# Performance work log

Hardware: AMD Instinct MI355X
Metric: run time of the kernel (lower is better)

## Reference

```python
import jax, jax.numpy as jnp
import numpy as np

N = 100000      # num_nodes
E = 1600000     # num_edges (avg degree 16)
D_IN, D_H, D_OUT = 128, 128, 64


def _glorot(key, shape):
    fan_in = shape[0]
    bound = 1.0 / np.sqrt(fan_in)
    return jax.random.uniform(key, shape, jnp.float32, -bound, bound)


def setup_inputs() -> dict:
    key = jax.random.key(0)
    ks = jax.random.split(key, 9)
    x = jax.random.normal(ks[0], (N, D_IN), jnp.float32)
    edge_index = jax.random.randint(ks[1], (2, E), 0, N, jnp.int32)
    # SAGEConv layer 1: lin_l (aggregated, with bias) and lin_r (root, no bias)
    W1l = _glorot(ks[2], (D_IN, D_H))
    b1 = jnp.zeros((D_H,), jnp.float32)
    W1r = _glorot(ks[3], (D_IN, D_H))
    # SAGEConv layer 2
    W2l = _glorot(ks[4], (D_H, D_OUT))
    b2 = jnp.zeros((D_OUT,), jnp.float32)
    W2r = _glorot(ks[5], (D_H, D_OUT))
    return {"x": x, "W1l": W1l, "b1": b1, "W1r": W1r,
            "W2l": W2l, "b2": b2, "W2r": W2r, "edge_index": edge_index}


def _sage_conv(x, edge_index, Wl, b, Wr):
    """PyG SAGEConv with mean aggregation: out = mean_{j in N(i)} x_j @ Wl + b + x_i @ Wr."""
    src, dst = edge_index[0], edge_index[1]
    msg_sum = jax.ops.segment_sum(x[src], dst, num_segments=N)          # [N, d_in]
    deg = jax.ops.segment_sum(jnp.ones((src.shape[0],), x.dtype), dst,
                              num_segments=N)                            # [N]
    mean = msg_sum / jnp.maximum(deg, 1.0)[:, None]
    return mean @ Wl + b + x @ Wr


def reference(x, W1l, b1, W1r, W2l, b2, W2r, edge_index):
    h = jax.nn.relu(_sage_conv(x, edge_index, W1l, b1, W1r))
    # dropout is identity at inference (training=False)
    return _sage_conv(h, edge_index, W2l, b2, W2r)
```

## Files before the change

### kernel.cpp

```cpp
#include <hip/hip_runtime.h>

#define NODES 100000
#define NEDGE 1600000
#define NPART 8
#define PSIZE (NODES / NPART)
#define EW 48

typedef _Float16 half8 __attribute__((ext_vector_type(8)));
typedef float floatx4 __attribute__((ext_vector_type(4)));
typedef float floatx2 __attribute__((ext_vector_type(2)));
typedef int intx4 __attribute__((ext_vector_type(4)));


static __device__ __forceinline__ unsigned int packh2(float a, float b) {
    union { _Float16 h; unsigned short s; } x, y;
    x.h = (_Float16)a; y.h = (_Float16)b;
    return (unsigned int)x.s | ((unsigned int)y.s << 16);
}
static __device__ __forceinline__ float2 unpackh2(unsigned int u) {
    union { unsigned short s; _Float16 h; } x, y;
    x.s = (unsigned short)(u & 0xffffu);
    y.s = (unsigned short)(u >> 16);
    return make_float2((float)x.h, (float)y.h);
}


template <bool HI>
static __device__ __forceinline__ float2 fp8x2_to_f32(unsigned int u) {
    floatx2 r = __builtin_amdgcn_cvt_pk_f32_fp8(u, HI);
    return make_float2(r.x, r.y);
}
static __device__ __forceinline__ unsigned int pack4fp8(float a, float b,
                                                        float c, float d) {
    unsigned int w = (unsigned int)__builtin_amdgcn_cvt_pk_fp8_f32(a, b, 0, false);
    w = (unsigned int)__builtin_amdgcn_cvt_pk_fp8_f32(c, d, (int)w, true);
    return w;
}


static __global__ __launch_bounds__(256) void prep_kernel(
    const float* __restrict__ W1l, const float* __restrict__ W1r,
    const float* __restrict__ W2l, const float* __restrict__ W2r,
    _Float16* __restrict__ WT1, _Float16* __restrict__ WT2,
    int* __restrict__ cnt) {
    int bid = blockIdx.x;
    if (bid < 192) {
        int idx = bid * 256 + threadIdx.x;
        if (idx < 256 * 128) {
            int n = idx >> 7, k = idx & 127;
            float v = (n < 128) ? W1l[k * 128 + n] : W1r[k * 128 + (n - 128)];
            WT1[n * 128 + k] = (_Float16)v;
        } else if (idx < 256 * 128 + 128 * 128) {
            int i2 = idx - 256 * 128;
            int n = i2 >> 7, k = i2 & 127;
            float v = (n < 64) ? W2l[k * 64 + n] : W2r[k * 64 + (n - 64)];
            WT2[n * 128 + k] = (_Float16)v;
        }
    } else {
        int i = (bid - 192) * 256 + threadIdx.x;
        int stride = 128 * 256;
        for (; i < NODES; i += stride) cnt[i] = 0;
    }
}


static __global__ __launch_bounds__(256) void build_ell_kernel(
    const int* __restrict__ src, const int* __restrict__ dst,
    int* __restrict__ cnt, int* __restrict__ colE) {
    const int part = blockIdx.x & (NPART - 1);
    const int lo = part * PSIZE;
    const int hi = lo + PSIZE;
    const int group = blockIdx.x >> 3;
    const int ngroups = gridDim.x >> 3;
    const int NV = NEDGE / 4;
    const intx4* dst4 = (const intx4*)dst;
    const intx4* src4 = (const intx4*)src;
    int i = group * 256 + threadIdx.x;
    int stride = ngroups * 256;
    for (int e4 = i; e4 < NV; e4 += stride) {
        intx4 d4 = __builtin_nontemporal_load(dst4 + e4);
        intx4 s4 = __builtin_nontemporal_load(src4 + e4);
#pragma unroll
        for (int q = 0; q < 4; ++q) {
            int d = d4[q];
            if (d >= lo && d < hi) {
                int pos = atomicAdd(&cnt[d], 1);
                if (pos < EW) colE[(size_t)d * EW + pos] = s4[q];
            }
        }
    }
}


static __global__ __launch_bounds__(256) void gemm1_mfma_kernel(
    const float* __restrict__ X, const _Float16* __restrict__ WT1,
    const float* __restrict__ b1,
    unsigned char* __restrict__ U8, _Float16* __restrict__ V16) {
    __shared__ _Float16 sX[64][136];
    const int tid = threadIdx.x;
    const int row0 = blockIdx.x * 64;
    {
        int c4 = (tid & 31) * 4;
        int r0 = tid >> 5;
#pragma unroll
        for (int p = 0; p < 8; ++p) {
            int r = r0 + p * 8;
            int row = row0 + r;
            float4 v = make_float4(0.f, 0.f, 0.f, 0.f);
            if (row < NODES) v = *(const float4*)(X + (size_t)row * 128 + c4);
            sX[r][c4 + 0] = (_Float16)v.x;
            sX[r][c4 + 1] = (_Float16)v.y;
            sX[r][c4 + 2] = (_Float16)v.z;
            sX[r][c4 + 3] = (_Float16)v.w;
        }
    }
    __syncthreads();

    const int wave = tid >> 6;
    const int lane = tid & 63;
    const int l15 = lane & 15;
    const int quad = lane >> 4;

    floatx4 acc[4][4];
#pragma unroll
    for (int j = 0; j < 4; ++j)
#pragma unroll
        for (int m = 0; m < 4; ++m) acc[j][m] = (floatx4){0.f, 0.f, 0.f, 0.f};

    const _Float16* Wbase = WT1 + (size_t)(wave * 64 + l15) * 128 + quad * 8;

    for (int k0 = 0; k0 < 128; k0 += 32) {
        half8 a[4];
#pragma unroll
        for (int m = 0; m < 4; ++m)
            a[m] = *(const half8*)&sX[m * 16 + l15][quad * 8 + k0];
#pragma unroll
        for (int j = 0; j < 4; ++j) {
            half8 b = *(const half8*)(Wbase + (size_t)j * 16 * 128 + k0);
#pragma unroll
            for (int m = 0; m < 4; ++m)
                acc[j][m] = __builtin_amdgcn_mfma_f32_16x16x32_f16(b, a[m], acc[j][m], 0, 0, 0);
        }
    }

    if (wave < 2) {
#pragma unroll
        for (int j = 0; j < 4; ++j) {
            int n0 = wave * 64 + j * 16 + quad * 4;
#pragma unroll
            for (int m = 0; m < 4; ++m) {
                int node = row0 + m * 16 + l15;
                if (node < NODES) {
                    unsigned int w = pack4fp8(acc[j][m][0], acc[j][m][1],
                                              acc[j][m][2], acc[j][m][3]);
                    *(unsigned int*)(U8 + (size_t)node * 128 + n0) = w;
                }
            }
        }
    } else {
#pragma unroll
        for (int j = 0; j < 4; ++j) {
            int nn0 = (wave - 2) * 64 + j * 16 + quad * 4;
            float4 bb = *(const float4*)(b1 + nn0);
#pragma unroll
            for (int m = 0; m < 4; ++m) {
                int node = row0 + m * 16 + l15;
                if (node < NODES) {
                    uint2 o;
                    o.x = packh2(acc[j][m][0] + bb.x, acc[j][m][1] + bb.y);
                    o.y = packh2(acc[j][m][2] + bb.z, acc[j][m][3] + bb.w);
                    *(uint2*)(V16 + (size_t)node * 128 + nn0) = o;
                }
            }
        }
    }
}


static __global__ __launch_bounds__(256) void agg1_kernel(
    const unsigned char* __restrict__ U8, const int* __restrict__ cnt,
    const int* __restrict__ colE, unsigned int* __restrict__ H32) {
    int node = (int)((blockIdx.x * 256 + threadIdx.x) >> 6);
    int lane = threadIdx.x & 63;
    if (node >= NODES) return;
    const int g = lane >> 4;
    const int l16 = lane & 15;
    int dcnt = cnt[node];
    if (dcnt > EW) dcnt = EW;
    int s = node * EW;
    int e = s + dcnt;
    float inv = 1.0f / (float)max(dcnt, 1);

    float acc[8];
#pragma unroll
    for (int i = 0; i < 8; ++i) acc[i] = 0.f;

    int p = s + g;
    for (; p + 12 < e; p += 16) {
        int c0 = colE[p], c1 = colE[p + 4], c2 = colE[p + 8], c3 = colE[p + 12];
        uint2 u0 = *(const uint2*)(U8 + (size_t)c0 * 128 + l16 * 8);
        uint2 u1 = *(const uint2*)(U8 + (size_t)c1 * 128 + l16 * 8);
        uint2 u2 = *(const uint2*)(U8 + (size_t)c2 * 128 + l16 * 8);
        uint2 u3 = *(const uint2*)(U8 + (size_t)c3 * 128 + l16 * 8);
#pragma unroll
        for (int q = 0; q < 4; ++q) {
            uint2 u = (q == 0) ? u0 : (q == 1) ? u1 : (q == 2) ? u2 : u3;
            float2 a0 = fp8x2_to_f32<false>(u.x), a1 = fp8x2_to_f32<true>(u.x);
            float2 a2 = fp8x2_to_f32<false>(u.y), a3 = fp8x2_to_f32<true>(u.y);
            acc[0] += a0.x; acc[1] += a0.y; acc[2] += a1.x; acc[3] += a1.y;
            acc[4] += a2.x; acc[5] += a2.y; acc[6] += a3.x; acc[7] += a3.y;
        }
    }
    for (; p < e; p += 4) {
        uint2 u = *(const uint2*)(U8 + (size_t)colE[p] * 128 + l16 * 8);
        float2 a0 = fp8x2_to_f32<false>(u.x), a1 = fp8x2_to_f32<true>(u.x);
        float2 a2 = fp8x2_to_f32<false>(u.y), a3 = fp8x2_to_f32<true>(u.y);
        acc[0] += a0.x; acc[1] += a0.y; acc[2] += a1.x; acc[3] += a1.y;
        acc[4] += a2.x; acc[5] += a2.y; acc[6] += a3.x; acc[7] += a3.y;
    }

#pragma unroll
    for (int i = 0; i < 8; ++i) {
        acc[i] += __shfl_xor(acc[i], 16);
        acc[i] += __shfl_xor(acc[i], 32);
    }

    if (lane < 16) {
        uint4 vv = *(const uint4*)(H32 + (size_t)node * 64 + l16 * 4);
        float2 v0 = unpackh2(vv.x), v1 = unpackh2(vv.y);
        float2 v2 = unpackh2(vv.z), v3 = unpackh2(vv.w);
        uint4 o;
        o.x = packh2(fmaxf(acc[0] * inv + v0.x, 0.f), fmaxf(acc[1] * inv + v0.y, 0.f));
        o.y = packh2(fmaxf(acc[2] * inv + v1.x, 0.f), fmaxf(acc[3] * inv + v1.y, 0.f));
        o.z = packh2(fmaxf(acc[4] * inv + v2.x, 0.f), fmaxf(acc[5] * inv + v2.y, 0.f));
        o.w = packh2(fmaxf(acc[6] * inv + v3.x, 0.f), fmaxf(acc[7] * inv + v3.y, 0.f));
        *(uint4*)(H32 + (size_t)node * 64 + l16 * 4) = o;
    }
}


static __global__ __launch_bounds__(256) void gemm2_mfma_kernel(
    const _Float16* __restrict__ H16, const _Float16* __restrict__ WT2,
    const float* __restrict__ b2,
    _Float16* __restrict__ T16, float* __restrict__ OUT) {
    __shared__ _Float16 sX[64][136];
    const int tid = threadIdx.x;
    const int row0 = blockIdx.x * 64;
    {
        int c8 = (tid & 15) * 8;
        int r0 = tid >> 4;
#pragma unroll
        for (int p = 0; p < 4; ++p) {
            int r = r0 + p * 16;
            int row = row0 + r;
            uint4 v = make_uint4(0u, 0u, 0u, 0u);
            if (row < NODES) v = *(const uint4*)(H16 + (size_t)row * 128 + c8);
            *(uint4*)&sX[r][c8] = v;
        }
    }
    __syncthreads();

    const int wave = tid >> 6;
    const int lane = tid & 63;
    const int l15 = lane & 15;
    const int quad = lane >> 4;

    floatx4 acc[2][4];
#pragma unroll
    for (int j = 0; j < 2; ++j)
#pragma unroll
        for (int m = 0; m < 4; ++m) acc[j][m] = (floatx4){0.f, 0.f, 0.f, 0.f};

    const _Float16* Wbase = WT2 + (size_t)(wave * 32 + l15) * 128 + quad * 8;

    for (int k0 = 0; k0 < 128; k0 += 32) {
        half8 a[4];
#pragma unroll
        for (int m = 0; m < 4; ++m)
            a[m] = *(const half8*)&sX[m * 16 + l15][quad * 8 + k0];
#pragma unroll
        for (int j = 0; j < 2; ++j) {
            half8 b = *(const half8*)(Wbase + (size_t)j * 16 * 128 + k0);
#pragma unroll
            for (int m = 0; m < 4; ++m)
                acc[j][m] = __builtin_amdgcn_mfma_f32_16x16x32_f16(b, a[m], acc[j][m], 0, 0, 0);
        }
    }

    const bool isOut = (wave >= 2);
#pragma unroll
    for (int j = 0; j < 2; ++j) {
        int n0 = wave * 32 + j * 16 + quad * 4;
        if (isOut) {
            int nn0 = n0 - 64;
            float4 bb = *(const float4*)(b2 + nn0);
#pragma unroll
            for (int m = 0; m < 4; ++m) {
                int node = row0 + m * 16 + l15;
                if (node < NODES) {
                    float4 o = make_float4(acc[j][m][0] + bb.x, acc[j][m][1] + bb.y,
                                           acc[j][m][2] + bb.z, acc[j][m][3] + bb.w);
                    *(float4*)(OUT + (size_t)node * 64 + nn0) = o;
                }
            }
        } else {
#pragma unroll
            for (int m = 0; m < 4; ++m) {
                int node = row0 + m * 16 + l15;
                if (node < NODES) {
                    uint2 o;
                    o.x = packh2(acc[j][m][0], acc[j][m][1]);
                    o.y = packh2(acc[j][m][2], acc[j][m][3]);
                    *(uint2*)(T16 + (size_t)node * 64 + n0) = o;
                }
            }
        }
    }
}


static __global__ __launch_bounds__(256) void agg2_kernel(
    const unsigned int* __restrict__ T32, const int* __restrict__ cnt,
    const int* __restrict__ colE, float* __restrict__ OUT) {
    int node = (int)((blockIdx.x * 256 + threadIdx.x) >> 6);
    int lane = threadIdx.x & 63;
    if (node >= NODES) return;
    const int g = lane >> 4;
    const int l16 = lane & 15;
    int dcnt = cnt[node];
    if (dcnt > EW) dcnt = EW;
    int s = node * EW;
    int e = s + dcnt;
    float inv = 1.0f / (float)max(dcnt, 1);

    float acc[4];
#pragma unroll
    for (int i = 0; i < 4; ++i) acc[i] = 0.f;

    int p = s + g;
    for (; p + 12 < e; p += 16) {
        int c0 = colE[p], c1 = colE[p + 4], c2 = colE[p + 8], c3 = colE[p + 12];
        uint2 u0 = *(const uint2*)(T32 + (size_t)c0 * 32 + l16 * 2);
        uint2 u1 = *(const uint2*)(T32 + (size_t)c1 * 32 + l16 * 2);
        uint2 u2 = *(const uint2*)(T32 + (size_t)c2 * 32 + l16 * 2);
        uint2 u3 = *(const uint2*)(T32 + (size_t)c3 * 32 + l16 * 2);
#pragma unroll
        for (int q = 0; q < 4; ++q) {
            uint2 u = (q == 0) ? u0 : (q == 1) ? u1 : (q == 2) ? u2 : u3;
            float2 a0 = unpackh2(u.x), a1 = unpackh2(u.y);
            acc[0] += a0.x; acc[1] += a0.y; acc[2] += a1.x; acc[3] += a1.y;
        }
    }
    for (; p < e; p += 4) {
        uint2 u = *(const uint2*)(T32 + (size_t)colE[p] * 32 + l16 * 2);
        float2 a0 = unpackh2(u.x), a1 = unpackh2(u.y);
        acc[0] += a0.x; acc[1] += a0.y; acc[2] += a1.x; acc[3] += a1.y;
    }

#pragma unroll
    for (int i = 0; i < 4; ++i) {
        acc[i] += __shfl_xor(acc[i], 16);
        acc[i] += __shfl_xor(acc[i], 32);
    }

    if (lane < 16) {
        float4 o = *(float4*)(OUT + (size_t)node * 64 + l16 * 4);
        o.x += acc[0] * inv;
        o.y += acc[1] * inv;
        o.z += acc[2] * inv;
        o.w += acc[3] * inv;
        *(float4*)(OUT + (size_t)node * 64 + l16 * 4) = o;
    }
}


extern "C" void kernel_launch(void* const* d_in, const int* in_sizes, int n_in,
                              void* d_out, int out_size, void* d_ws, size_t ws_size,
                              hipStream_t stream) {
    const float* x   = (const float*)d_in[0];
    const float* W1l = (const float*)d_in[1];
    const float* b1  = (const float*)d_in[2];
    const float* W1r = (const float*)d_in[3];
    const float* W2l = (const float*)d_in[4];
    const float* b2  = (const float*)d_in[5];
    const float* W2r = (const float*)d_in[6];
    const int*   ei  = (const int*)d_in[7];
    const int* esrc = ei;
    const int* edst = ei + NEDGE;
    float* out = (float*)d_out;

    char* ws = (char*)d_ws;
    size_t off = 0;
    int* colE     = (int*)(ws + off); off += (size_t)NODES * EW * 4;
    unsigned char* U8 = (unsigned char*)(ws + off); off += (size_t)NODES * 128;
    _Float16* V16 = (_Float16*)(ws + off); off += (size_t)NODES * 128 * 2;
    int* cnt      = (int*)(ws + off); off += (((size_t)NODES * 4) + 255) & ~(size_t)255;
    _Float16* WT1 = (_Float16*)(ws + off); off += 256 * 128 * 2;
    _Float16* WT2 = (_Float16*)(ws + off); off += 128 * 128 * 2;
    _Float16* T16 = (_Float16*)U8;

    const int gemm_grid = (NODES + 63) / 64;
    const int agg_grid  = (NODES + 3) / 4;

    prep_kernel<<<320, 256, 0, stream>>>(W1l, W1r, W2l, W2r, WT1, WT2, cnt);
    build_ell_kernel<<<2048, 256, 0, stream>>>(esrc, edst, cnt, colE);

    gemm1_mfma_kernel<<<gemm_grid, 256, 0, stream>>>(x, WT1, b1, U8, V16);
    agg1_kernel<<<agg_grid, 256, 0, stream>>>(U8, cnt, colE, (unsigned int*)V16);

    gemm2_mfma_kernel<<<gemm_grid, 256, 0, stream>>>(V16, WT2, b2, T16, out);
    agg2_kernel<<<agg_grid, 256, 0, stream>>>(
        (const unsigned int*)T16, cnt, colE, out);
}
```

Baseline: 343.5 us.

## Split ELL build into two launches with scalar loads and lazy src reads

The ELL build kernel is split into two launches, each covering half the edge list. It now reads one edge per thread with scalar loads and only fetches the source index when the destination falls in the block's partition, which avoids reading src for 7/8 of the edges. The gemm1 staging also packs the four fp16 values into a single 8-byte shared store instead of four separate half stores. The scalar loads give up 16-byte vectorized access, and the second launch adds launch overhead.

```diff
diff --git a/kernel.cpp b/kernel.cpp
--- a/kernel.cpp
+++ b/kernel.cpp
@@ -9,7 +9,6 @@
 typedef _Float16 half8 __attribute__((ext_vector_type(8)));
 typedef float floatx4 __attribute__((ext_vector_type(4)));
 typedef float floatx2 __attribute__((ext_vector_type(2)));
-typedef int intx4 __attribute__((ext_vector_type(4)));
 
 
 static __device__ __forceinline__ unsigned int packh2(float a, float b) {
@@ -66,27 +65,21 @@
 
 static __global__ __launch_bounds__(256) void build_ell_kernel(
     const int* __restrict__ src, const int* __restrict__ dst,
-    int* __restrict__ cnt, int* __restrict__ colE) {
+    int* __restrict__ cnt, int* __restrict__ colE,
+    int ebase, int eend) {
     const int part = blockIdx.x & (NPART - 1);
     const int lo = part * PSIZE;
     const int hi = lo + PSIZE;
     const int group = blockIdx.x >> 3;
     const int ngroups = gridDim.x >> 3;
-    const int NV = NEDGE / 4;
-    const intx4* dst4 = (const intx4*)dst;
-    const intx4* src4 = (const intx4*)src;
     int i = group * 256 + threadIdx.x;
     int stride = ngroups * 256;
-    for (int e4 = i; e4 < NV; e4 += stride) {
-        intx4 d4 = __builtin_nontemporal_load(dst4 + e4);
-        intx4 s4 = __builtin_nontemporal_load(src4 + e4);
-#pragma unroll
-        for (int q = 0; q < 4; ++q) {
-            int d = d4[q];
-            if (d >= lo && d < hi) {
-                int pos = atomicAdd(&cnt[d], 1);
-                if (pos < EW) colE[(size_t)d * EW + pos] = s4[q];
-            }
+    for (int e = ebase + i; e < eend; e += stride) {
+        int d = __builtin_nontemporal_load(dst + e);
+        if (d >= lo && d < hi) {
+            int sv = __builtin_nontemporal_load(src + e);
+            int pos = atomicAdd(&cnt[d], 1);
+            if (pos < EW) colE[(size_t)d * EW + pos] = sv;
         }
     }
 }
@@ -108,10 +101,10 @@
             int row = row0 + r;
             float4 v = make_float4(0.f, 0.f, 0.f, 0.f);
             if (row < NODES) v = *(const float4*)(X + (size_t)row * 128 + c4);
-            sX[r][c4 + 0] = (_Float16)v.x;
-            sX[r][c4 + 1] = (_Float16)v.y;
-            sX[r][c4 + 2] = (_Float16)v.z;
-            sX[r][c4 + 3] = (_Float16)v.w;
+            uint2 o;
+            o.x = packh2(v.x, v.y);
+            o.y = packh2(v.z, v.w);
+            *(uint2*)&sX[r][c4] = o;
         }
     }
     __syncthreads();
@@ -403,7 +396,10 @@
     const int agg_grid  = (NODES + 3) / 4;
 
     prep_kernel<<<320, 256, 0, stream>>>(W1l, W1r, W2l, W2r, WT1, WT2, cnt);
-    build_ell_kernel<<<2048, 256, 0, stream>>>(esrc, edst, cnt, colE);
+    build_ell_kernel<<<1024, 256, 0, stream>>>(esrc, edst, cnt, colE,
+                                               0, NEDGE / 2);
+    build_ell_kernel<<<1024, 256, 0, stream>>>(esrc, edst, cnt, colE,
+                                               NEDGE / 2, NEDGE);
 
     gemm1_mfma_kernel<<<gemm_grid, 256, 0, stream>>>(x, WT1, b1, U8, V16);
     agg1_kernel<<<agg_grid, 256, 0, stream>>>(U8, cnt, colE, (unsigned int*)V16);
```

Result: slower. 372.0 us (+8.3%).
